# Kernel tuning notes

Hardware: AMD Instinct MI355X
Metric: run time of the kernel (lower is better)

## Reference

```python
import jax, jax.numpy as jnp
import numpy as np

N_NODES = 50000
N_EDGES = 800000
FEAT = 128
HID1 = 128
HID2 = 64


def setup_inputs() -> dict:
    key = jax.random.key(0)
    k = jax.random.split(key, 6)
    x = jax.random.normal(k[0], (N_NODES, FEAT), dtype=jnp.float32)
    edge_index = jax.random.randint(k[1], (2, N_EDGES), 0, N_NODES, dtype=jnp.int32)
    # Glorot-style init scaling like PyG's GCNConv linear
    W1 = jax.random.normal(k[2], (FEAT, HID1), dtype=jnp.float32) * (1.0 / np.sqrt(FEAT))
    b1 = jnp.zeros((HID1,), dtype=jnp.float32)
    W2 = jax.random.normal(k[3], (HID1, HID2), dtype=jnp.float32) * (1.0 / np.sqrt(HID1))
    b2 = jnp.zeros((HID2,), dtype=jnp.float32)
    return {"x": x, "edge_index": edge_index, "W1": W1, "b1": b1, "W2": W2, "b2": b2}


def _gcn_conv(x, src, dst, W, b, n_nodes):
    """PyG GCNConv: h = X W; out_i = sum_j norm_ij h_j + b, with self-loops and
    symmetric normalization norm_ij = deg_i^-1/2 * deg_j^-1/2 (deg counts self-loop)."""
    h = x @ W  # [N, out]
    # degree at target nodes (self-loops already appended to src/dst)
    deg = jax.ops.segment_sum(jnp.ones_like(dst, dtype=h.dtype), dst, num_segments=n_nodes)
    dinv = jax.lax.rsqrt(jnp.maximum(deg, 1.0))  # deg >= 1 because of self-loops
    norm = dinv[src] * dinv[dst]  # [E+N]
    msg = h[src] * norm[:, None]  # gather + scale, [E+N, out]
    out = jax.ops.segment_sum(msg, dst, num_segments=n_nodes)
    return out + b


def reference(x, edge_index, W1, b1, W2, b2):
    n = x.shape[0]
    self_idx = jnp.arange(n, dtype=edge_index.dtype)
    src = jnp.concatenate([edge_index[0], self_idx])
    dst = jnp.concatenate([edge_index[1], self_idx])
    h = jax.nn.relu(_gcn_conv(x, src, dst, W1, b1, n))
    out = _gcn_conv(h, src, dst, W2, b2, n)
    return out
```

## Files before the change

### kernel.cpp

```cpp
#include <hip/hip_runtime.h>
#include <hip/hip_bf16.h>


typedef __attribute__((ext_vector_type(8))) short short8;
typedef __attribute__((ext_vector_type(4))) float f32x4;

__device__ __forceinline__ float bf_lo(unsigned u) { return __uint_as_float(u << 16); }
__device__ __forceinline__ float bf_hi(unsigned u) { return __uint_as_float(u & 0xffff0000u); }
__device__ __forceinline__ unsigned short f2bf(float f) {
    return (unsigned short)(__bfloat16_as_ushort(__float2bfloat16(f)));
}

__global__ __launch_bounds__(256) void zero_kernel(int* __restrict__ a, int n) {
    int i = blockIdx.x * 256 + threadIdx.x;
    if (i < n) a[i] = 0;
}

__global__ __launch_bounds__(256) void count_kernel(const int* __restrict__ dst,
                                                    int* __restrict__ cnt,
                                                    int* __restrict__ eslot, int E) {
    int e = blockIdx.x * 256 + threadIdx.x;
    if (e < E) eslot[e] = atomicAdd(&cnt[dst[e]], 1);
}

__global__ __launch_bounds__(256) void scan1_kernel(const int* __restrict__ cnt,
                                                    int* __restrict__ row_ptr,
                                                    int* __restrict__ blksum,
                                                    float* __restrict__ dinv, int N) {
    __shared__ int sm[256];
    int i = blockIdx.x * 256 + threadIdx.x;
    int v = (i < N) ? cnt[i] : 0;
    if (i < N) dinv[i] = rsqrtf((float)(v + 1));
    sm[threadIdx.x] = v;
    __syncthreads();
    for (int off = 1; off < 256; off <<= 1) {
        int t = (threadIdx.x >= off) ? sm[threadIdx.x - off] : 0;
        __syncthreads();
        sm[threadIdx.x] += t;
        __syncthreads();
    }
    if (i < N) row_ptr[i] = sm[threadIdx.x] - v;
    if (threadIdx.x == 255) blksum[blockIdx.x] = sm[255];
}

__global__ __launch_bounds__(256) void scan2_kernel(int* __restrict__ blksum, int nb) {
    __shared__ int sm[256];
    int i = threadIdx.x;
    int v = (i < nb) ? blksum[i] : 0;
    sm[i] = v;
    __syncthreads();
    for (int off = 1; off < 256; off <<= 1) {
        int t = (i >= off) ? sm[i - off] : 0;
        __syncthreads();
        sm[i] += t;
        __syncthreads();
    }
    if (i < nb) blksum[i] = sm[i] - v;
}

__global__ __launch_bounds__(256) void scan3_kernel(int* __restrict__ row_ptr,
                                                    const int* __restrict__ blksum,
                                                    int N, int E) {
    int i = blockIdx.x * 256 + threadIdx.x;
    if (i < N) row_ptr[i] += blksum[blockIdx.x];
    if (i == 0) row_ptr[N] = E;
}

__global__ __launch_bounds__(256) void scatter_kernel(const int* __restrict__ src,
                                                      const int* __restrict__ dst,
                                                      const int* __restrict__ row_ptr,
                                                      const int* __restrict__ eslot,
                                                      int* __restrict__ ssrc, int E) {
    int e = blockIdx.x * 256 + threadIdx.x;
    if (e < E) {
        int p = row_ptr[dst[e]] + eslot[e];
        ssrc[p] = src[e];
    }
}

__global__ __launch_bounds__(256) void packw_kernel(const float* __restrict__ W,
                                                    unsigned short* __restrict__ Wp,
                                                    int ncol) {
    int i = blockIdx.x * 256 + threadIdx.x;
    if (i < 128 * ncol) {
        int j = i & 7;
        int n = (i >> 3) % ncol;
        int kb = i / (8 * ncol);
        Wp[i] = f2bf(W[(kb * 8 + j) * ncol + n]);
    }
}

template <int M, bool ABF16>
__global__ __launch_bounds__(256) void mfma_gemm_kernel(const void* __restrict__ Araw,
                                                        const unsigned short* __restrict__ Wp,
                                                        const float* __restrict__ dinv,
                                                        unsigned short* __restrict__ C,
                                                        int N) {
    constexpr int NT = M / 16;
    const int lane = threadIdx.x & 63;
    const int wave = threadIdx.x >> 6;
    const int col = lane & 15;
    const int quad = lane >> 4;
    const int row0w = (blockIdx.x * 4 + wave) * 16;

    int arow = row0w + col;
    if (arow >= N) arow = N - 1;

    short8 afr[4];
    if constexpr (!ABF16) {
        const float* Xr = (const float*)Araw + (size_t)arow * 128;
#pragma unroll
        for (int c = 0; c < 4; ++c) {
            float4 f0 = *(const float4*)(Xr + c * 32 + quad * 8);
            float4 f1 = *(const float4*)(Xr + c * 32 + quad * 8 + 4);
            short8 a;
            a[0] = (short)f2bf(f0.x); a[1] = (short)f2bf(f0.y);
            a[2] = (short)f2bf(f0.z); a[3] = (short)f2bf(f0.w);
            a[4] = (short)f2bf(f1.x); a[5] = (short)f2bf(f1.y);
            a[6] = (short)f2bf(f1.z); a[7] = (short)f2bf(f1.w);
            afr[c] = a;
        }
    } else {
        const uint4* Z = (const uint4*)Araw;
#pragma unroll
        for (int c = 0; c < 4; ++c) {
            union { uint4 u; short8 s; } cv;
            cv.u = Z[(size_t)arow * 16 + c * 4 + quad];
            afr[c] = cv.s;
        }
    }

    f32x4 acc[NT];
#pragma unroll
    for (int t = 0; t < NT; ++t) acc[t] = (f32x4){0.f, 0.f, 0.f, 0.f};

    const uint4* Wq = (const uint4*)Wp;
#pragma unroll
    for (int c = 0; c < 4; ++c) {
        short8 bfr[NT];
#pragma unroll
        for (int t = 0; t < NT; ++t) {
            union { uint4 u; short8 s; } cv;
            cv.u = Wq[(size_t)(c * 4 + quad) * M + t * 16 + col];
            bfr[t] = cv.s;
        }
#pragma unroll
        for (int t = 0; t < NT; ++t)
            acc[t] = __builtin_amdgcn_mfma_f32_16x16x32_bf16(afr[c], bfr[t], acc[t], 0, 0, 0);
    }

#pragma unroll
    for (int r = 0; r < 4; ++r) {
        int row = row0w + quad * 4 + r;
        if (row < N) {
            float dv = dinv[row];
#pragma unroll
            for (int t = 0; t < NT; ++t)
                C[(size_t)row * M + t * 16 + col] = f2bf(acc[t][r] * dv);
        }
    }
}

template <int M, bool RELU, bool OUTBF16>
__global__ __launch_bounds__(256) void agg_kernel(const unsigned short* __restrict__ g,
                                                  const int* __restrict__ row_ptr,
                                                  const int* __restrict__ ssrc,
                                                  const float* __restrict__ dinv,
                                                  const float* __restrict__ bias,
                                                  void* __restrict__ outraw, int N) {
    int node = __builtin_amdgcn_readfirstlane((int)(blockIdx.x * 4 + (threadIdx.x >> 6)));
    if (node >= N) return;
    int lane = threadIdx.x & 63;
    float di = dinv[node];
    int beg = row_ptr[node];
    int end = row_ptr[node + 1];

    if constexpr (M == 128) {
        const unsigned* hp = (const unsigned*)g;
        unsigned hv = hp[node * 64 + lane];
        float ax0 = bf_lo(hv), ay0 = bf_hi(hv);
        float ax1 = 0.f, ay1 = 0.f;
        int j = beg;
        for (; j + 7 < end; j += 8) {
            int s0 = ssrc[j + 0], s1 = ssrc[j + 1], s2 = ssrc[j + 2], s3 = ssrc[j + 3];
            int s4 = ssrc[j + 4], s5 = ssrc[j + 5], s6 = ssrc[j + 6], s7 = ssrc[j + 7];
            unsigned v0 = hp[s0 * 64 + lane], v1 = hp[s1 * 64 + lane];
            unsigned v2 = hp[s2 * 64 + lane], v3 = hp[s3 * 64 + lane];
            unsigned v4 = hp[s4 * 64 + lane], v5 = hp[s5 * 64 + lane];
            unsigned v6 = hp[s6 * 64 + lane], v7 = hp[s7 * 64 + lane];
            ax0 += bf_lo(v0) + bf_lo(v1) + bf_lo(v2) + bf_lo(v3);
            ax1 += bf_lo(v4) + bf_lo(v5) + bf_lo(v6) + bf_lo(v7);
            ay0 += bf_hi(v0) + bf_hi(v1) + bf_hi(v2) + bf_hi(v3);
            ay1 += bf_hi(v4) + bf_hi(v5) + bf_hi(v6) + bf_hi(v7);
        }
        for (; j + 3 < end; j += 4) {
            int s0 = ssrc[j + 0], s1 = ssrc[j + 1], s2 = ssrc[j + 2], s3 = ssrc[j + 3];
            unsigned v0 = hp[s0 * 64 + lane], v1 = hp[s1 * 64 + lane];
            unsigned v2 = hp[s2 * 64 + lane], v3 = hp[s3 * 64 + lane];
            ax0 += bf_lo(v0) + bf_lo(v1);
            ax1 += bf_lo(v2) + bf_lo(v3);
            ay0 += bf_hi(v0) + bf_hi(v1);
            ay1 += bf_hi(v2) + bf_hi(v3);
        }
        for (; j < end; ++j) {
            unsigned v = hp[ssrc[j] * 64 + lane];
            ax0 += bf_lo(v);
            ay0 += bf_hi(v);
        }
        float ax = (ax0 + ax1) * di + bias[2 * lane];
        float ay = (ay0 + ay1) * di + bias[2 * lane + 1];
        if (RELU) { ax = fmaxf(ax, 0.f); ay = fmaxf(ay, 0.f); }
        if constexpr (OUTBF16) {
            unsigned pk = (unsigned)f2bf(ax) | ((unsigned)f2bf(ay) << 16);
            ((unsigned*)outraw)[node * 64 + lane] = pk;
        } else {
            ((float2*)outraw)[node * 64 + lane] = make_float2(ax, ay);
        }
    } else {
        float a0 = __uint_as_float((unsigned)g[node * 64 + lane] << 16);
        float a1 = 0.f;
        int j = beg;
        for (; j + 7 < end; j += 8) {
            int s0 = ssrc[j + 0], s1 = ssrc[j + 1], s2 = ssrc[j + 2], s3 = ssrc[j + 3];
            int s4 = ssrc[j + 4], s5 = ssrc[j + 5], s6 = ssrc[j + 6], s7 = ssrc[j + 7];
            float v0 = __uint_as_float((unsigned)g[s0 * 64 + lane] << 16);
            float v1 = __uint_as_float((unsigned)g[s1 * 64 + lane] << 16);
            float v2 = __uint_as_float((unsigned)g[s2 * 64 + lane] << 16);
            float v3 = __uint_as_float((unsigned)g[s3 * 64 + lane] << 16);
            float v4 = __uint_as_float((unsigned)g[s4 * 64 + lane] << 16);
            float v5 = __uint_as_float((unsigned)g[s5 * 64 + lane] << 16);
            float v6 = __uint_as_float((unsigned)g[s6 * 64 + lane] << 16);
            float v7 = __uint_as_float((unsigned)g[s7 * 64 + lane] << 16);
            a0 += v0 + v1 + v2 + v3;
            a1 += v4 + v5 + v6 + v7;
        }
        for (; j + 3 < end; j += 4) {
            int s0 = ssrc[j + 0], s1 = ssrc[j + 1], s2 = ssrc[j + 2], s3 = ssrc[j + 3];
            float v0 = __uint_as_float((unsigned)g[s0 * 64 + lane] << 16);
            float v1 = __uint_as_float((unsigned)g[s1 * 64 + lane] << 16);
            float v2 = __uint_as_float((unsigned)g[s2 * 64 + lane] << 16);
            float v3 = __uint_as_float((unsigned)g[s3 * 64 + lane] << 16);
            a0 += v0 + v1;
            a1 += v2 + v3;
        }
        for (; j < end; ++j)
            a0 += __uint_as_float((unsigned)g[ssrc[j] * 64 + lane] << 16);
        float acc = (a0 + a1) * di + bias[lane];
        if (RELU) acc = fmaxf(acc, 0.f);
        if constexpr (OUTBF16) {
            ((unsigned short*)outraw)[node * 64 + lane] = f2bf(acc);
        } else {
            ((float*)outraw)[node * 64 + lane] = acc;
        }
    }
}

extern "C" void kernel_launch(void* const* d_in, const int* in_sizes, int n_in,
                              void* d_out, int out_size, void* d_ws, size_t ws_size,
                              hipStream_t stream) {
    const float* x = (const float*)d_in[0];
    const int* eidx = (const int*)d_in[1];
    const float* W1 = (const float*)d_in[2];
    const float* b1 = (const float*)d_in[3];
    const float* W2 = (const float*)d_in[4];
    const float* b2 = (const float*)d_in[5];
    float* out = (float*)d_out;

    const int N = in_sizes[0] / 128;
    const int E = in_sizes[1] / 2;
    const int* src = eidx;
    const int* dst = eidx + E;

    char* ws = (char*)d_ws;
    size_t off = 0;
    auto alloc = [&](size_t bytes) -> char* {
        char* p = ws + off;
        off = (off + bytes + 255) & ~(size_t)255;
        return p;
    };
    int* cnt = (int*)alloc((size_t)N * 4);
    int* row_ptr = (int*)alloc((size_t)(N + 1) * 4);
    int* blksum = (int*)alloc(256 * 4);
    int* eslot = (int*)alloc((size_t)E * 4);
    int* ssrc = (int*)alloc((size_t)E * 4);
    float* dinv = (float*)alloc((size_t)N * 4);
    unsigned short* Wp1 = (unsigned short*)alloc(128 * 128 * 2);
    unsigned short* Wp2 = (unsigned short*)alloc(128 * 64 * 2);
    unsigned short* g1 = (unsigned short*)alloc((size_t)N * 128 * 2);
    unsigned short* z1 = (unsigned short*)alloc((size_t)N * 128 * 2);
    unsigned short* g2 = (unsigned short*)alloc((size_t)N * 64 * 2);

    const int nbN = (N + 255) / 256;
    const int nbE = (E + 255) / 256;

    zero_kernel<<<nbN, 256, 0, stream>>>(cnt, N);
    count_kernel<<<nbE, 256, 0, stream>>>(dst, cnt, eslot, E);
    scan1_kernel<<<nbN, 256, 0, stream>>>(cnt, row_ptr, blksum, dinv, N);
    scan2_kernel<<<1, 256, 0, stream>>>(blksum, nbN);
    scan3_kernel<<<nbN, 256, 0, stream>>>(row_ptr, blksum, N, E);
    scatter_kernel<<<nbE, 256, 0, stream>>>(src, dst, row_ptr, eslot, ssrc, E);

    packw_kernel<<<(128 * 128 + 255) / 256, 256, 0, stream>>>(W1, Wp1, 128);
    packw_kernel<<<(128 * 64 + 255) / 256, 256, 0, stream>>>(W2, Wp2, 64);

    const int gb = (N + 63) / 64;
    mfma_gemm_kernel<128, false><<<gb, 256, 0, stream>>>(x, Wp1, dinv, g1, N);
    agg_kernel<128, true, true><<<(N + 3) / 4, 256, 0, stream>>>(g1, row_ptr, ssrc, dinv, b1, z1, N);
    mfma_gemm_kernel<64, true><<<gb, 256, 0, stream>>>(z1, Wp2, dinv, g2, N);
    agg_kernel<64, false, false><<<(N + 3) / 4, 256, 0, stream>>>(g2, row_ptr, ssrc, dinv, b2, out, N);
}
```

Before: 210.5 us.

## Merge setup, scan and scatter+GEMM kernels to cut launch count

Folds the count-buffer zeroing and both weight packs into one setup kernel. It replaces the three-kernel block scan with a single 1024-thread chunked scan that also computes dinv, and merges the edge scatter with the first-layer GEMM into one launch split by block index. The aim is to remove kernel launch gaps and small-kernel overhead, cutting the launch count from 12 to 7. The trade-off is a single-block scan whose threads walk strided, uncoalesced chunks of about 49 elements each, which could become a serial bottleneck.

```diff
diff --git a/kernel.cpp b/kernel.cpp
--- a/kernel.cpp
+++ b/kernel.cpp
@@ -11,9 +11,27 @@
     return (unsigned short)(__bfloat16_as_ushort(__float2bfloat16(f)));
 }
 
-__global__ __launch_bounds__(256) void zero_kernel(int* __restrict__ a, int n) {
+__global__ __launch_bounds__(256) void setup_kernel(int* __restrict__ cnt, int N,
+                                                    const float* __restrict__ W1,
+                                                    unsigned short* __restrict__ Wp1,
+                                                    const float* __restrict__ W2,
+                                                    unsigned short* __restrict__ Wp2) {
     int i = blockIdx.x * 256 + threadIdx.x;
-    if (i < n) a[i] = 0;
+    if (i < N) {
+        cnt[i] = 0;
+    } else if (i < N + 128 * 128) {
+        int q = i - N;
+        int j = q & 7;
+        int n = (q >> 3) & 127;
+        int kb = q >> 10;
+        Wp1[q] = f2bf(W1[(kb * 8 + j) * 128 + n]);
+    } else if (i < N + 128 * 128 + 128 * 64) {
+        int q = i - N - 128 * 128;
+        int j = q & 7;
+        int n = (q >> 3) & 63;
+        int kb = q >> 9;
+        Wp2[q] = f2bf(W2[(kb * 8 + j) * 64 + n]);
+    }
 }
 
 __global__ __launch_bounds__(256) void count_kernel(const int* __restrict__ dst,
@@ -23,75 +41,124 @@
     if (e < E) eslot[e] = atomicAdd(&cnt[dst[e]], 1);
 }
 
-__global__ __launch_bounds__(256) void scan1_kernel(const int* __restrict__ cnt,
+__global__ __launch_bounds__(1024) void scan_kernel(const int* __restrict__ cnt,
                                                     int* __restrict__ row_ptr,
-                                                    int* __restrict__ blksum,
-                                                    float* __restrict__ dinv, int N) {
-    __shared__ int sm[256];
-    int i = blockIdx.x * 256 + threadIdx.x;
-    int v = (i < N) ? cnt[i] : 0;
-    if (i < N) dinv[i] = rsqrtf((float)(v + 1));
-    sm[threadIdx.x] = v;
+                                                    float* __restrict__ dinv,
+                                                    int N, int E) {
+    __shared__ int sm[1024];
+    const int t = threadIdx.x;
+    const int CH = (N + 1023) / 1024;
+    const int lo = t * CH;
+    const int hi = min(lo + CH, N);
+
+    int s = 0;
+    for (int i = lo; i < hi; ++i) s += cnt[i];
+    sm[t] = s;
     __syncthreads();
-    for (int off = 1; off < 256; off <<= 1) {
-        int t = (threadIdx.x >= off) ? sm[threadIdx.x - off] : 0;
-        __syncthreads();
-        sm[threadIdx.x] += t;
-        __syncthreads();
-    }
-    if (i < N) row_ptr[i] = sm[threadIdx.x] - v;
-    if (threadIdx.x == 255) blksum[blockIdx.x] = sm[255];
-}
-
-__global__ __launch_bounds__(256) void scan2_kernel(int* __restrict__ blksum, int nb) {
-    __shared__ int sm[256];
-    int i = threadIdx.x;
-    int v = (i < nb) ? blksum[i] : 0;
-    sm[i] = v;
+
+    if (t < 64) {
+        int base = t * 16;
+        int run = 0;
+#pragma unroll
+        for (int k = 0; k < 16; ++k) {
+            int c = sm[base + k];
+            sm[base + k] = run;
+            run += c;
+        }
+        int v = run;
+#pragma unroll
+        for (int off = 1; off < 64; off <<= 1) {
+            int u = __shfl_up(v, off, 64);
+            if (t >= off) v += u;
+        }
+        int gex = v - run;
+#pragma unroll
+        for (int k = 0; k < 16; ++k) sm[base + k] += gex;
+    }
     __syncthreads();
-    for (int off = 1; off < 256; off <<= 1) {
-        int t = (i >= off) ? sm[i - off] : 0;
-        __syncthreads();
-        sm[i] += t;
-        __syncthreads();
-    }
-    if (i < nb) blksum[i] = sm[i] - v;
-}
-
-__global__ __launch_bounds__(256) void scan3_kernel(int* __restrict__ row_ptr,
-                                                    const int* __restrict__ blksum,
-                                                    int N, int E) {
-    int i = blockIdx.x * 256 + threadIdx.x;
-    if (i < N) row_ptr[i] += blksum[blockIdx.x];
-    if (i == 0) row_ptr[N] = E;
-}
-
-__global__ __launch_bounds__(256) void scatter_kernel(const int* __restrict__ src,
-                                                      const int* __restrict__ dst,
-                                                      const int* __restrict__ row_ptr,
-                                                      const int* __restrict__ eslot,
-                                                      int* __restrict__ ssrc, int E) {
-    int e = blockIdx.x * 256 + threadIdx.x;
-    if (e < E) {
-        int p = row_ptr[dst[e]] + eslot[e];
-        ssrc[p] = src[e];
-    }
-}
-
-__global__ __launch_bounds__(256) void packw_kernel(const float* __restrict__ W,
-                                                    unsigned short* __restrict__ Wp,
-                                                    int ncol) {
-    int i = blockIdx.x * 256 + threadIdx.x;
-    if (i < 128 * ncol) {
-        int j = i & 7;
-        int n = (i >> 3) % ncol;
-        int kb = i / (8 * ncol);
-        Wp[i] = f2bf(W[(kb * 8 + j) * ncol + n]);
-    }
-}
-
-template <int M, bool ABF16>
-__global__ __launch_bounds__(256) void mfma_gemm_kernel(const void* __restrict__ Araw,
+
+    int run = sm[t];
+    for (int i = lo; i < hi; ++i) {
+        int c = cnt[i];
+        row_ptr[i] = run;
+        dinv[i] = rsqrtf((float)(c + 1));
+        run += c;
+    }
+    if (t == 0) row_ptr[N] = E;
+}
+
+__global__ __launch_bounds__(256) void scatgemm_kernel(
+    const int* __restrict__ src, const int* __restrict__ dst,
+    const int* __restrict__ row_ptr, const int* __restrict__ eslot,
+    int* __restrict__ ssrc, int E,
+    const float* __restrict__ X, const unsigned short* __restrict__ Wp1,
+    const float* __restrict__ dinv, unsigned short* __restrict__ g1,
+    int N, int gb) {
+    if ((int)blockIdx.x >= gb) {
+        int e = (blockIdx.x - gb) * 256 + threadIdx.x;
+        if (e < E) {
+            int p = row_ptr[dst[e]] + eslot[e];
+            ssrc[p] = src[e];
+        }
+        return;
+    }
+    constexpr int NT = 8;
+    const int lane = threadIdx.x & 63;
+    const int wave = threadIdx.x >> 6;
+    const int col = lane & 15;
+    const int quad = lane >> 4;
+    const int row0w = (blockIdx.x * 4 + wave) * 16;
+
+    int arow = row0w + col;
+    if (arow >= N) arow = N - 1;
+
+    short8 afr[4];
+    const float* Xr = X + (size_t)arow * 128;
+#pragma unroll
+    for (int c = 0; c < 4; ++c) {
+        float4 f0 = *(const float4*)(Xr + c * 32 + quad * 8);
+        float4 f1 = *(const float4*)(Xr + c * 32 + quad * 8 + 4);
+        short8 a;
+        a[0] = (short)f2bf(f0.x); a[1] = (short)f2bf(f0.y);
+        a[2] = (short)f2bf(f0.z); a[3] = (short)f2bf(f0.w);
+        a[4] = (short)f2bf(f1.x); a[5] = (short)f2bf(f1.y);
+        a[6] = (short)f2bf(f1.z); a[7] = (short)f2bf(f1.w);
+        afr[c] = a;
+    }
+
+    f32x4 acc[NT];
+#pragma unroll
+    for (int t = 0; t < NT; ++t) acc[t] = (f32x4){0.f, 0.f, 0.f, 0.f};
+
+    const uint4* Wq = (const uint4*)Wp1;
+#pragma unroll
+    for (int c = 0; c < 4; ++c) {
+        short8 bfr[NT];
+#pragma unroll
+        for (int t = 0; t < NT; ++t) {
+            union { uint4 u; short8 s; } cv;
+            cv.u = Wq[(size_t)(c * 4 + quad) * 128 + t * 16 + col];
+            bfr[t] = cv.s;
+        }
+#pragma unroll
+        for (int t = 0; t < NT; ++t)
+            acc[t] = __builtin_amdgcn_mfma_f32_16x16x32_bf16(afr[c], bfr[t], acc[t], 0, 0, 0);
+    }
+
+#pragma unroll
+    for (int r = 0; r < 4; ++r) {
+        int row = row0w + quad * 4 + r;
+        if (row < N) {
+            float dv = dinv[row];
+#pragma unroll
+            for (int t = 0; t < NT; ++t)
+                g1[(size_t)row * 128 + t * 16 + col] = f2bf(acc[t][r] * dv);
+        }
+    }
+}
+
+template <int M>
+__global__ __launch_bounds__(256) void mfma_gemm_kernel(const unsigned short* __restrict__ A,
                                                         const unsigned short* __restrict__ Wp,
                                                         const float* __restrict__ dinv,
                                                         unsigned short* __restrict__ C,
@@ -107,27 +174,12 @@
     if (arow >= N) arow = N - 1;
 
     short8 afr[4];
-    if constexpr (!ABF16) {
-        const float* Xr = (const float*)Araw + (size_t)arow * 128;
-#pragma unroll
-        for (int c = 0; c < 4; ++c) {
-            float4 f0 = *(const float4*)(Xr + c * 32 + quad * 8);
-            float4 f1 = *(const float4*)(Xr + c * 32 + quad * 8 + 4);
-            short8 a;
-            a[0] = (short)f2bf(f0.x); a[1] = (short)f2bf(f0.y);
-            a[2] = (short)f2bf(f0.z); a[3] = (short)f2bf(f0.w);
-            a[4] = (short)f2bf(f1.x); a[5] = (short)f2bf(f1.y);
-            a[6] = (short)f2bf(f1.z); a[7] = (short)f2bf(f1.w);
-            afr[c] = a;
-        }
-    } else {
-        const uint4* Z = (const uint4*)Araw;
-#pragma unroll
-        for (int c = 0; c < 4; ++c) {
-            union { uint4 u; short8 s; } cv;
-            cv.u = Z[(size_t)arow * 16 + c * 4 + quad];
-            afr[c] = cv.s;
-        }
+    const uint4* Z = (const uint4*)A;
+#pragma unroll
+    for (int c = 0; c < 4; ++c) {
+        union { uint4 u; short8 s; } cv;
+        cv.u = Z[(size_t)arow * 16 + c * 4 + quad];
+        afr[c] = cv.s;
     }
 
     f32x4 acc[NT];
@@ -280,7 +332,6 @@
     };
     int* cnt = (int*)alloc((size_t)N * 4);
     int* row_ptr = (int*)alloc((size_t)(N + 1) * 4);
-    int* blksum = (int*)alloc(256 * 4);
     int* eslot = (int*)alloc((size_t)E * 4);
     int* ssrc = (int*)alloc((size_t)E * 4);
     float* dinv = (float*)alloc((size_t)N * 4);
@@ -290,22 +341,16 @@
     unsigned short* z1 = (unsigned short*)alloc((size_t)N * 128 * 2);
     unsigned short* g2 = (unsigned short*)alloc((size_t)N * 64 * 2);
 
-    const int nbN = (N + 255) / 256;
     const int nbE = (E + 255) / 256;
-
-    zero_kernel<<<nbN, 256, 0, stream>>>(cnt, N);
+    const int gb = (N + 63) / 64;
+    const int setup_n = N + 128 * 128 + 128 * 64;
+
+    setup_kernel<<<(setup_n + 255) / 256, 256, 0, stream>>>(cnt, N, W1, Wp1, W2, Wp2);
     count_kernel<<<nbE, 256, 0, stream>>>(dst, cnt, eslot, E);
-    scan1_kernel<<<nbN, 256, 0, stream>>>(cnt, row_ptr, blksum, dinv, N);
-    scan2_kernel<<<1, 256, 0, stream>>>(blksum, nbN);
-    scan3_kernel<<<nbN, 256, 0, stream>>>(row_ptr, blksum, N, E);
-    scatter_kernel<<<nbE, 256, 0, stream>>>(src, dst, row_ptr, eslot, ssrc, E);
-
-    packw_kernel<<<(128 * 128 + 255) / 256, 256, 0, stream>>>(W1, Wp1, 128);
-    packw_kernel<<<(128 * 64 + 255) / 256, 256, 0, stream>>>(W2, Wp2, 64);
-
-    const int gb = (N + 63) / 64;
-    mfma_gemm_kernel<128, false><<<gb, 256, 0, stream>>>(x, Wp1, dinv, g1, N);
+    scan_kernel<<<1, 1024, 0, stream>>>(cnt, row_ptr, dinv, N, E);
+    scatgemm_kernel<<<gb + nbE, 256, 0, stream>>>(src, dst, row_ptr, eslot, ssrc, E,
+                                                  x, Wp1, dinv, g1, N, gb);
     agg_kernel<128, true, true><<<(N + 3) / 4, 256, 0, stream>>>(g1, row_ptr, ssrc, dinv, b1, z1, N);
-    mfma_gemm_kernel<64, true><<<gb, 256, 0, stream>>>(z1, Wp2, dinv, g2, N);
+    mfma_gemm_kernel<64><<<gb, 256, 0, stream>>>(z1, Wp2, dinv, g2, N);
     agg_kernel<64, false, false><<<(N + 3) / 4, 256, 0, stream>>>(g2, row_ptr, ssrc, dinv, b2, out, N);
 }
```

Result: slower. 295.3 us (+40.3%).
